# Kernel tuning notes

Hardware: AMD Instinct MI355X
Metric: run time of the kernel (lower is better)

The kernel has to match this reference:

```python
import jax, jax.numpy as jnp
import numpy as np

N = 512      # hidden states
M = 32000    # observation vocab
B = 64       # batch
TMAX = 256   # max sequence length


def setup_inputs() -> dict:
    key = jax.random.key(0)
    k1, k2, k3, k4, k5 = jax.random.split(key, 5)
    return {
        "x": jax.random.randint(k1, (B, TMAX), 0, M),          # observations
        "T": jax.random.randint(k2, (B,), 1, TMAX + 1),        # lengths in [1, TMAX]
        "trans": jax.random.normal(k3, (N, N), dtype=jnp.float32),  # unnormalized transition
        "emis": jax.random.normal(k4, (N, M), dtype=jnp.float32),   # unnormalized emission
        "prior": jax.random.normal(k5, (N,), dtype=jnp.float32),    # unnormalized state priors
    }


def reference(x, T, trans, emis, prior):
    # columns of transition matrix sum to 1 (log_softmax over dim=0 in torch)
    log_A = jax.nn.log_softmax(trans, axis=0)    # (N, N): log_A[j, k] = log p(z_t=j | z_{t-1}=k)
    log_E = jax.nn.log_softmax(emis, axis=1)     # (N, M)
    log_pi = jax.nn.log_softmax(prior, axis=0)   # (N,)

    # emission log-probs for every timestep, gathered once: (B, TMAX, N)
    em = log_E.T[x]

    alpha0 = em[:, 0, :] + log_pi                # (B, N)

    def step(alpha, em_t):
        # out[b, j] = em_t[b, j] + logsumexp_k (log_A[j, k] + alpha[b, k])
        new = em_t + jax.nn.logsumexp(alpha[:, None, :] + log_A[None, :, :], axis=2)
        return new, new

    _, alphas = jax.lax.scan(step, alpha0, jnp.swapaxes(em[:, 1:, :], 0, 1))  # (TMAX-1, B, N)
    log_alpha = jnp.concatenate([alpha0[:, None, :], jnp.swapaxes(alphas, 0, 1)], axis=1)  # (B, TMAX, N)

    log_sums = jax.nn.logsumexp(log_alpha, axis=2)                       # (B, TMAX)
    log_probs = jnp.take_along_axis(log_sums, (T - 1)[:, None], axis=1)  # (B, 1)
    return log_probs
```

## Files before the change

### kernel.cpp

```cpp
#include <hip/hip_runtime.h>
#include <math.h>

#define Nn 512
#define Mm 32000
#define Bb 64
#define Tt 256
#define NCONS 4
#define NPROD 128

typedef float v4f __attribute__((ext_vector_type(4)));
typedef float f4  __attribute__((ext_vector_type(4)));
typedef int   v4i __attribute__((ext_vector_type(4)));
typedef int   v8i __attribute__((ext_vector_type(8)));

__device__ inline int pk4fp8(float a, float b, float c, float d) {
  int r = __builtin_amdgcn_cvt_pk_fp8_f32(a, b, 0, false);
  r = __builtin_amdgcn_cvt_pk_fp8_f32(c, d, r, true);
  return r;
}

__global__ void k_colsum(const float* __restrict__ trans, float* __restrict__ colsum) {
  int tid = threadIdx.x;
  int j0 = blockIdx.x * 16;
  float a0 = 0.f, a1 = 0.f;
  for (int r = 0; r < 16; ++r) {
    a0 += __expf(trans[(j0 + r) * Nn + tid]);
    a1 += __expf(trans[(j0 + r) * Nn + 256 + tid]);
  }
  atomicAdd(&colsum[tid], a0);
  atomicAdd(&colsum[256 + tid], a1);
}

__global__ void k_writeA8(const float* __restrict__ trans, const float* __restrict__ colsum,
                          int* __restrict__ A8) {
  int d = blockIdx.x * 256 + threadIdx.x;
  int j = d >> 7, k0 = (d & 127) << 2;
  float v0 = 256.f * __expf(trans[j * Nn + k0 + 0]) / colsum[k0 + 0];
  float v1 = 256.f * __expf(trans[j * Nn + k0 + 1]) / colsum[k0 + 1];
  float v2 = 256.f * __expf(trans[j * Nn + k0 + 2]) / colsum[k0 + 2];
  float v3 = 256.f * __expf(trans[j * Nn + k0 + 3]) / colsum[k0 + 3];
  A8[d] = pk4fp8(v0, v1, v2, v3);
}

__global__ __attribute__((amdgpu_flat_work_group_size(512, 512), amdgpu_waves_per_eu(2, 2)))
void k_fused(
    const char* __restrict__ A8, const float* __restrict__ emis,
    const int* __restrict__ x, const float* __restrict__ prior,
    const int* __restrict__ Tlen, float* __restrict__ Pem2,
    int* __restrict__ progress, float* __restrict__ out)
{
  __shared__ __align__(16) char ybuf[2][16 * Nn];
  __shared__ __align__(16) float ss[512];
  __shared__ __align__(16) f4 ss4[512];
  const int tid = threadIdx.x;

  if (blockIdx.x >= NCONS) {
    const int p = blockIdx.x - NCONS;
    const int j0 = p * 4;

    float e = __expf(prior[tid]);
    ss[tid] = e; __syncthreads();
    for (int off = 256; off; off >>= 1) { if (tid < off) ss[tid] += ss[tid + off]; __syncthreads(); }
    const float ptot = ss[0];

    const f4* q0 = (const f4*)(emis + (size_t)(j0 + 0) * Mm);
    const f4* q1 = (const f4*)(emis + (size_t)(j0 + 1) * Mm);
    const f4* q2 = (const f4*)(emis + (size_t)(j0 + 2) * Mm);
    const f4* q3 = (const f4*)(emis + (size_t)(j0 + 3) * Mm);
    f4 a4 = {0.f, 0.f, 0.f, 0.f};
    for (int i = tid; i < Mm / 4; i += 512) {
      f4 v0 = q0[i], v1 = q1[i], v2 = q2[i], v3 = q3[i];
      a4[0] += (__expf(v0[0]) + __expf(v0[1])) + (__expf(v0[2]) + __expf(v0[3]));
      a4[1] += (__expf(v1[0]) + __expf(v1[1])) + (__expf(v1[2]) + __expf(v1[3]));
      a4[2] += (__expf(v2[0]) + __expf(v2[1])) + (__expf(v2[2]) + __expf(v2[3]));
      a4[3] += (__expf(v3[0]) + __expf(v3[1])) + (__expf(v3[2]) + __expf(v3[3]));
    }
    ss4[tid] = a4; __syncthreads();
    for (int off = 256; off; off >>= 1) { if (tid < off) ss4[tid] += ss4[tid + off]; __syncthreads(); }
    f4 tot = ss4[0];
    f4 rs, fz;
    #pragma unroll
    for (int q = 0; q < 4; ++q) {
      rs[q] = 32768.f / tot[q];
      fz[q] = rs[q] * 256.f * __expf(prior[j0 + q]) / ptot;
    }

    const float* r0 = emis + (size_t)(j0 + 0) * Mm;
    const float* r1 = emis + (size_t)(j0 + 1) * Mm;
    const float* r2 = emis + (size_t)(j0 + 2) * Mm;
    const float* r3 = emis + (size_t)(j0 + 3) * Mm;
    f4* P4 = (f4*)Pem2;
    for (int c8 = 0; c8 < 8; ++c8) {
      #pragma unroll
      for (int r = 0; r < 4; ++r) {
        int idx = c8 * 2048 + r * 512 + tid;
        int t = idx >> 6, b = idx & 63;
        int mv = x[b * Tt + t];
        f4 fq = (t == 0) ? fz : rs;
        f4 o = { __expf(r0[mv]) * fq[0], __expf(r1[mv]) * fq[1],
                 __expf(r2[mv]) * fq[2], __expf(r3[mv]) * fq[3] };
        P4[t * 8192 + (b >> 4) * 2048 + p * 16 + (b & 15)] = o;
      }
      __syncthreads();
      if (tid == 0) {
        __builtin_amdgcn_fence(__ATOMIC_RELEASE, "agent");
        __hip_atomic_fetch_add(&progress[c8], 1, __ATOMIC_RELAXED, __HIP_MEMORY_SCOPE_AGENT);
      }
    }
    return;
  }

  const int g = blockIdx.x;
  const int w = tid >> 6, lane = tid & 63;
  const int c = lane & 15, kq = lane >> 4;
  const int jw = w * 64;
  const int swz = (c & 7) << 4;
  const int b = g * 16 + c;

  v8i af[4][4];
  #pragma unroll
  for (int rt = 0; rt < 4; ++rt)
    #pragma unroll
    for (int kc = 0; kc < 4; ++kc)
      af[rt][kc] = *reinterpret_cast<const v8i*>(
          A8 + (size_t)(jw + rt * 16 + c) * Nn + kc * 128 + kq * 32);

  v8i onesv;
  #pragma unroll
  for (int u = 0; u < 8; ++u) onesv[u] = 0x38383838;

  #pragma unroll
  for (int rt = 0; rt < 4; ++rt)
    #pragma unroll
    for (int kc = 0; kc < 4; ++kc)
      asm volatile("" : "+v"(af[rt][kc]));
  asm volatile("" : "+v"(onesv));

  const int Tb = Tlen[b];
  int E = 23;
  int csafe = 0;

  #define ENSURE(NEED)                                                                      \
    while (csafe <= (NEED)) {                                                               \
      if (__hip_atomic_load(&progress[csafe], __ATOMIC_RELAXED,                             \
                            __HIP_MEMORY_SCOPE_AGENT) >= NPROD) {                           \
        ++csafe;                                                                            \
        __builtin_amdgcn_fence(__ATOMIC_ACQUIRE, "agent");                                  \
      } else __builtin_amdgcn_s_sleep(2);                                                   \
    }

  const int roA0 = (c * Nn + kq * 32) ^ swz;
  const int roB0 = roA0 ^ 16;
  const int wf0 = (c * Nn + jw + kq * 4) ^ swz;
  const int wf1 = wf0 ^ 16, wf2 = wf0 ^ 32, wf3 = wf0 ^ 48;
  char* const yb0 = &ybuf[0][0];

  const char* rdA_e = yb0 + roA0;
  const char* rdB_e = yb0 + roB0;
  const char* rdA_o = rdA_e + 8192;
  const char* rdB_o = rdB_e + 8192;
  char* const wb_o = yb0 + 8192;
  char* const wb_e = yb0;

  ENSURE(0);

  {
    int cc = tid & 15, grp = tid >> 4, jb = grp * 16, sz = (cc & 7) << 4;
    const f4* P0 = (const f4*)Pem2 + g * 2048 + (jb >> 2) * 16 + cc;
    #pragma unroll
    for (int q = 0; q < 4; ++q) {
      f4 v = P0[q * 16];
      *reinterpret_cast<int*>(yb0 + ((cc * Nn + jb + q * 4) ^ sz)) = pk4fp8(v[0], v[1], v[2], v[3]);
    }
  }
  __syncthreads();

  const f4* pemP = (const f4*)Pem2 + (8192 + g * 2048 + jw * 4 + kq * 16 + c);

  union BU { v8i v; v4i h[2]; };

  #define LOADMFMA(RDA, RDB)                                                                 \
    BU b0, b1, b2, b3;                                                                       \
    b0.h[0] = *(const v4i*)((RDA) + 0);   b0.h[1] = *(const v4i*)((RDB) + 0);                \
    b1.h[0] = *(const v4i*)((RDA) + 128); b1.h[1] = *(const v4i*)((RDB) + 128);              \
    b2.h[0] = *(const v4i*)((RDA) + 256); b2.h[1] = *(const v4i*)((RDB) + 256);              \
    b3.h[0] = *(const v4i*)((RDA) + 384); b3.h[1] = *(const v4i*)((RDB) + 384);              \
    v4f a0 = {0.f,0.f,0.f,0.f}, a1 = {0.f,0.f,0.f,0.f};                                     \
    v4f a2 = {0.f,0.f,0.f,0.f}, a3 = {0.f,0.f,0.f,0.f};                                     \
    v4f as_ = {0.f,0.f,0.f,0.f};                                                            \
    as_ = __builtin_amdgcn_mfma_scale_f32_16x16x128_f8f6f4(onesv,    b0.v, as_, 0,0,0, 0x7F, 0, 0x7F); \
    a0  = __builtin_amdgcn_mfma_scale_f32_16x16x128_f8f6f4(af[0][0], b0.v, a0, 0,0,0, 0x7F, 0, 0x7F); \
    a1  = __builtin_amdgcn_mfma_scale_f32_16x16x128_f8f6f4(af[1][0], b0.v, a1, 0,0,0, 0x7F, 0, 0x7F); \
    a2  = __builtin_amdgcn_mfma_scale_f32_16x16x128_f8f6f4(af[2][0], b0.v, a2, 0,0,0, 0x7F, 0, 0x7F); \
    a3  = __builtin_amdgcn_mfma_scale_f32_16x16x128_f8f6f4(af[3][0], b0.v, a3, 0,0,0, 0x7F, 0, 0x7F); \
    as_ = __builtin_amdgcn_mfma_scale_f32_16x16x128_f8f6f4(onesv,    b1.v, as_, 0,0,0, 0x7F, 0, 0x7F); \
    a0  = __builtin_amdgcn_mfma_scale_f32_16x16x128_f8f6f4(af[0][1], b1.v, a0, 0,0,0, 0x7F, 0, 0x7F); \
    a1  = __builtin_amdgcn_mfma_scale_f32_16x16x128_f8f6f4(af[1][1], b1.v, a1, 0,0,0, 0x7F, 0, 0x7F); \
    a2  = __builtin_amdgcn_mfma_scale_f32_16x16x128_f8f6f4(af[2][1], b1.v, a2, 0,0,0, 0x7F, 0, 0x7F); \
    a3  = __builtin_amdgcn_mfma_scale_f32_16x16x128_f8f6f4(af[3][1], b1.v, a3, 0,0,0, 0x7F, 0, 0x7F); \
    as_ = __builtin_amdgcn_mfma_scale_f32_16x16x128_f8f6f4(onesv,    b2.v, as_, 0,0,0, 0x7F, 0, 0x7F); \
    a0  = __builtin_amdgcn_mfma_scale_f32_16x16x128_f8f6f4(af[0][2], b2.v, a0, 0,0,0, 0x7F, 0, 0x7F); \
    a1  = __builtin_amdgcn_mfma_scale_f32_16x16x128_f8f6f4(af[1][2], b2.v, a1, 0,0,0, 0x7F, 0, 0x7F); \
    a2  = __builtin_amdgcn_mfma_scale_f32_16x16x128_f8f6f4(af[2][2], b2.v, a2, 0,0,0, 0x7F, 0, 0x7F); \
    a3  = __builtin_amdgcn_mfma_scale_f32_16x16x128_f8f6f4(af[3][2], b2.v, a3, 0,0,0, 0x7F, 0, 0x7F); \
    as_ = __builtin_amdgcn_mfma_scale_f32_16x16x128_f8f6f4(onesv,    b3.v, as_, 0,0,0, 0x7F, 0, 0x7F); \
    a0  = __builtin_amdgcn_mfma_scale_f32_16x16x128_f8f6f4(af[0][3], b3.v, a0, 0,0,0, 0x7F, 0, 0x7F); \
    a1  = __builtin_amdgcn_mfma_scale_f32_16x16x128_f8f6f4(af[1][3], b3.v, a1, 0,0,0, 0x7F, 0, 0x7F); \
    a2  = __builtin_amdgcn_mfma_scale_f32_16x16x128_f8f6f4(af[2][3], b3.v, a2, 0,0,0, 0x7F, 0, 0x7F); \
    a3  = __builtin_amdgcn_mfma_scale_f32_16x16x128_f8f6f4(af[3][3], b3.v, a3, 0,0,0, 0x7F, 0, 0x7F);

  #define EPILOG(WBASE)                                                                      \
    {                                                                                        \
      v4f scl4 = {scl, scl, scl, scl};                                                       \
      v4f v0 = a0 * (pem0 * scl4);                                                           \
      v4f v1 = a1 * (pem1 * scl4);                                                           \
      v4f v2 = a2 * (pem2 * scl4);                                                           \
      v4f v3 = a3 * (pem3 * scl4);                                                           \
      *(int*)((WBASE) + wf0) = pk4fp8(v0[0], v0[1], v0[2], v0[3]);                           \
      *(int*)((WBASE) + wf1) = pk4fp8(v1[0], v1[1], v1[2], v1[3]);                           \
      *(int*)((WBASE) + wf2) = pk4fp8(v2[0], v2[1], v2[2], v2[3]);                           \
      *(int*)((WBASE) + wf3) = pk4fp8(v3[0], v3[1], v3[2], v3[3]);                           \
    }

  for (int t = 1; t <= Tt; t += 2) {
    {
      f4 pem0 = pemP[0], pem1 = pemP[64], pem2 = pemP[128], pem3 = pemP[192];
      LOADMFMA(rdA_e, rdB_e)
      float S = as_[0];
      int expb = (int)((__float_as_uint(S) >> 23) & 0xFF);
      if (w == 0 && kq == 0 && Tb == t) out[b] = __logf(S) - (float)E * 0.69314718056f;
      E += 150 - expb;
      float scl = __uint_as_float((unsigned)(254 - expb) << 23);
      EPILOG(wb_o)
      __syncthreads();
    }
    {
      const int T = t + 1;
      if (T < Tt && (T & 31) == 0) ENSURE(T >> 5);
      f4 pem0, pem1, pem2, pem3;
      const f4* p2 = pemP + 8192;
      if (T < Tt) { pem0 = p2[0]; pem1 = p2[64]; pem2 = p2[128]; pem3 = p2[192]; }
      LOADMFMA(rdA_o, rdB_o)
      float S = as_[0];
      int expb = (int)((__float_as_uint(S) >> 23) & 0xFF);
      if (w == 0 && kq == 0 && Tb == T) out[b] = __logf(S) - (float)E * 0.69314718056f;
      if (T == Tt) goto done;
      E += 150 - expb;
      float scl = __uint_as_float((unsigned)(254 - expb) << 23);
      EPILOG(wb_e)
      __syncthreads();
    }
    pemP += 16384;
  }
done: ;
  #undef LOADMFMA
  #undef EPILOG
  #undef ENSURE
}

extern "C" void kernel_launch(void* const* d_in, const int* in_sizes, int n_in,
                              void* d_out, int out_size, void* d_ws, size_t ws_size,
                              hipStream_t stream) {
  const int*   x     = (const int*)  d_in[0];
  const int*   Tlen  = (const int*)  d_in[1];
  const float* trans = (const float*)d_in[2];
  const float* emis  = (const float*)d_in[3];
  const float* prior = (const float*)d_in[4];
  float* out = (float*)d_out;

  char* w = (char*)d_ws;
  char*  A8       = (char*)(w);
  float* colsum   = (float*)(w + (512 << 10));
  int*   progress = (int*)  (w + (512 << 10) + 4096);
  float* Pem2     = (float*)(w + (1024 << 10));

  hipMemsetAsync(w + (512 << 10), 0, 8192, stream);
  k_colsum <<<32,  256, 0, stream>>>(trans, colsum);
  k_writeA8<<<256, 256, 0, stream>>>(trans, colsum, (int*)A8);
  k_fused  <<<NCONS + NPROD, 512, 0, stream>>>(A8, emis, x, prior, Tlen, Pem2, progress, out);
}
```

Measured before the change: 291.2 us.

## Fold emission row normalization into transition matrix and precompute in wide pre-kernel

Emission row sums are moved out of the 128 producer blocks into a separate 544-block pre-kernel that also computes the transition column sums. The emission normalization factor (1/rowsum) and the prior are folded into the FP8 transition matrix and into a small pi2 vector, so producers only compute raw exp(emis) gathers. This shortens the producer critical path before the consumers can start, at the cost of a full extra pass over the 65 MB emission matrix before the fused kernel launches. It also changes FP8 scaling, since the per-row factor now multiplies A rather than the emission term, which risks range or precision issues.

```diff
diff --git a/kernel.cpp b/kernel.cpp
--- a/kernel.cpp
+++ b/kernel.cpp
@@ -19,72 +19,69 @@
   return r;
 }
 
-__global__ void k_colsum(const float* __restrict__ trans, float* __restrict__ colsum) {
-  int tid = threadIdx.x;
-  int j0 = blockIdx.x * 16;
-  float a0 = 0.f, a1 = 0.f;
-  for (int r = 0; r < 16; ++r) {
-    a0 += __expf(trans[(j0 + r) * Nn + tid]);
-    a1 += __expf(trans[(j0 + r) * Nn + 256 + tid]);
-  }
-  atomicAdd(&colsum[tid], a0);
-  atomicAdd(&colsum[256 + tid], a1);
+__global__ void k_pre(const float* __restrict__ trans, const float* __restrict__ emis,
+                      float* __restrict__ colsum, float* __restrict__ rowsum) {
+  __shared__ float ss[256];
+  const int tid = threadIdx.x, bid = blockIdx.x;
+  if (bid < 512) {
+    const f4* row4 = (const f4*)(emis + (size_t)bid * Mm);
+    float s = 0.f;
+    for (int i = tid; i < Mm / 4; i += 256) {
+      f4 v = row4[i];
+      s += (__expf(v[0]) + __expf(v[1])) + (__expf(v[2]) + __expf(v[3]));
+    }
+    ss[tid] = s; __syncthreads();
+    for (int off = 128; off; off >>= 1) { if (tid < off) ss[tid] += ss[tid + off]; __syncthreads(); }
+    if (tid == 0) rowsum[bid] = ss[0];
+  } else {
+    int j0 = (bid - 512) * 16;
+    float a0 = 0.f, a1 = 0.f;
+    for (int r = 0; r < 16; ++r) {
+      a0 += __expf(trans[(j0 + r) * Nn + tid]);
+      a1 += __expf(trans[(j0 + r) * Nn + 256 + tid]);
+    }
+    atomicAdd(&colsum[tid], a0);
+    atomicAdd(&colsum[256 + tid], a1);
+  }
 }
 
 __global__ void k_writeA8(const float* __restrict__ trans, const float* __restrict__ colsum,
-                          int* __restrict__ A8) {
-  int d = blockIdx.x * 256 + threadIdx.x;
+                          const float* __restrict__ rowsum, const float* __restrict__ prior,
+                          int* __restrict__ A8, float* __restrict__ pi2) {
+  const int tid = threadIdx.x;
+  if (blockIdx.x == 256) {
+    __shared__ float ss[256];
+    float e0 = __expf(prior[tid]), e1 = __expf(prior[tid + 256]);
+    ss[tid] = e0 + e1; __syncthreads();
+    for (int off = 128; off; off >>= 1) { if (tid < off) ss[tid] += ss[tid + off]; __syncthreads(); }
+    float ptot = ss[0];
+    pi2[tid]       = 8388608.f * e0 / (ptot * rowsum[tid]);
+    pi2[tid + 256] = 8388608.f * e1 / (ptot * rowsum[tid + 256]);
+    return;
+  }
+  int d = blockIdx.x * 256 + tid;
   int j = d >> 7, k0 = (d & 127) << 2;
-  float v0 = 256.f * __expf(trans[j * Nn + k0 + 0]) / colsum[k0 + 0];
-  float v1 = 256.f * __expf(trans[j * Nn + k0 + 1]) / colsum[k0 + 1];
-  float v2 = 256.f * __expf(trans[j * Nn + k0 + 2]) / colsum[k0 + 2];
-  float v3 = 256.f * __expf(trans[j * Nn + k0 + 3]) / colsum[k0 + 3];
+  float f = 8388608.f / rowsum[j];
+  float v0 = f * __expf(trans[j * Nn + k0 + 0]) / colsum[k0 + 0];
+  float v1 = f * __expf(trans[j * Nn + k0 + 1]) / colsum[k0 + 1];
+  float v2 = f * __expf(trans[j * Nn + k0 + 2]) / colsum[k0 + 2];
+  float v3 = f * __expf(trans[j * Nn + k0 + 3]) / colsum[k0 + 3];
   A8[d] = pk4fp8(v0, v1, v2, v3);
 }
 
 __global__ __attribute__((amdgpu_flat_work_group_size(512, 512), amdgpu_waves_per_eu(2, 2)))
 void k_fused(
     const char* __restrict__ A8, const float* __restrict__ emis,
-    const int* __restrict__ x, const float* __restrict__ prior,
+    const int* __restrict__ x, const float* __restrict__ pi2,
     const int* __restrict__ Tlen, float* __restrict__ Pem2,
     int* __restrict__ progress, float* __restrict__ out)
 {
   __shared__ __align__(16) char ybuf[2][16 * Nn];
-  __shared__ __align__(16) float ss[512];
-  __shared__ __align__(16) f4 ss4[512];
   const int tid = threadIdx.x;
 
   if (blockIdx.x >= NCONS) {
     const int p = blockIdx.x - NCONS;
     const int j0 = p * 4;
-
-    float e = __expf(prior[tid]);
-    ss[tid] = e; __syncthreads();
-    for (int off = 256; off; off >>= 1) { if (tid < off) ss[tid] += ss[tid + off]; __syncthreads(); }
-    const float ptot = ss[0];
-
-    const f4* q0 = (const f4*)(emis + (size_t)(j0 + 0) * Mm);
-    const f4* q1 = (const f4*)(emis + (size_t)(j0 + 1) * Mm);
-    const f4* q2 = (const f4*)(emis + (size_t)(j0 + 2) * Mm);
-    const f4* q3 = (const f4*)(emis + (size_t)(j0 + 3) * Mm);
-    f4 a4 = {0.f, 0.f, 0.f, 0.f};
-    for (int i = tid; i < Mm / 4; i += 512) {
-      f4 v0 = q0[i], v1 = q1[i], v2 = q2[i], v3 = q3[i];
-      a4[0] += (__expf(v0[0]) + __expf(v0[1])) + (__expf(v0[2]) + __expf(v0[3]));
-      a4[1] += (__expf(v1[0]) + __expf(v1[1])) + (__expf(v1[2]) + __expf(v1[3]));
-      a4[2] += (__expf(v2[0]) + __expf(v2[1])) + (__expf(v2[2]) + __expf(v2[3]));
-      a4[3] += (__expf(v3[0]) + __expf(v3[1])) + (__expf(v3[2]) + __expf(v3[3]));
-    }
-    ss4[tid] = a4; __syncthreads();
-    for (int off = 256; off; off >>= 1) { if (tid < off) ss4[tid] += ss4[tid + off]; __syncthreads(); }
-    f4 tot = ss4[0];
-    f4 rs, fz;
-    #pragma unroll
-    for (int q = 0; q < 4; ++q) {
-      rs[q] = 32768.f / tot[q];
-      fz[q] = rs[q] * 256.f * __expf(prior[j0 + q]) / ptot;
-    }
-
     const float* r0 = emis + (size_t)(j0 + 0) * Mm;
     const float* r1 = emis + (size_t)(j0 + 1) * Mm;
     const float* r2 = emis + (size_t)(j0 + 2) * Mm;
@@ -96,9 +93,7 @@
         int idx = c8 * 2048 + r * 512 + tid;
         int t = idx >> 6, b = idx & 63;
         int mv = x[b * Tt + t];
-        f4 fq = (t == 0) ? fz : rs;
-        f4 o = { __expf(r0[mv]) * fq[0], __expf(r1[mv]) * fq[1],
-                 __expf(r2[mv]) * fq[2], __expf(r3[mv]) * fq[3] };
+        f4 o = { __expf(r0[mv]), __expf(r1[mv]), __expf(r2[mv]), __expf(r3[mv]) };
         P4[t * 8192 + (b >> 4) * 2048 + p * 16 + (b & 15)] = o;
       }
       __syncthreads();
@@ -167,9 +162,10 @@
   {
     int cc = tid & 15, grp = tid >> 4, jb = grp * 16, sz = (cc & 7) << 4;
     const f4* P0 = (const f4*)Pem2 + g * 2048 + (jb >> 2) * 16 + cc;
+    const f4* PI = (const f4*)pi2 + (jb >> 2);
     #pragma unroll
     for (int q = 0; q < 4; ++q) {
-      f4 v = P0[q * 16];
+      f4 v = P0[q * 16] * PI[q];
       *reinterpret_cast<int*>(yb0 + ((cc * Nn + jb + q * 4) ^ sz)) = pk4fp8(v[0], v[1], v[2], v[3]);
     }
   }
@@ -271,11 +267,13 @@
   char* w = (char*)d_ws;
   char*  A8       = (char*)(w);
   float* colsum   = (float*)(w + (512 << 10));
-  int*   progress = (int*)  (w + (512 << 10) + 4096);
+  float* rowsum   = (float*)(w + (512 << 10) + 2048);
+  float* pi2      = (float*)(w + (512 << 10) + 4096);
+  int*   progress = (int*)  (w + (512 << 10) + 8192);
   float* Pem2     = (float*)(w + (1024 << 10));
 
-  hipMemsetAsync(w + (512 << 10), 0, 8192, stream);
-  k_colsum <<<32,  256, 0, stream>>>(trans, colsum);
-  k_writeA8<<<256, 256, 0, stream>>>(trans, colsum, (int*)A8);
-  k_fused  <<<NCONS + NPROD, 512, 0, stream>>>(A8, emis, x, prior, Tlen, Pem2, progress, out);
-}
+  hipMemsetAsync(w + (512 << 10), 0, 12288, stream);
+  k_pre    <<<544, 256, 0, stream>>>(trans, emis, colsum, rowsum);
+  k_writeA8<<<257, 256, 0, stream>>>(trans, colsum, rowsum, prior, (int*)A8, pi2);
+  k_fused  <<<NCONS + NPROD, 512, 0, stream>>>(A8, emis, x, pi2, Tlen, Pem2, progress, out);
+}
```

After: 295.9 us. About the same (+1.6%).

## Fuse normalization prep into one kernel and fold emission normalization into transitions

Applied to the files above, without the earlier changes.

Drops the separate column-sum and FP8 transition-writing kernels and launches a single kernel with extra prep blocks. These blocks compute the transition column sums and the emission row sums in parallel and signal completion through progress counters. Producers now write unnormalized emission probabilities. Consumers wait for the prep counters, then build the FP8 transition fragments directly in registers, folding the per-row emission normalization into the transition rows; the t=0 term is scaled separately using the prior. This removes two launches and the A8 global round-trip. The cost is that consumers spin until all 412 prep blocks finish, and correctness relies on the grid being scheduled so those blocks eventually run.

```diff
diff --git a/kernel.cpp b/kernel.cpp
--- a/kernel.cpp
+++ b/kernel.cpp
@@ -7,6 +7,7 @@
 #define Tt 256
 #define NCONS 4
 #define NPROD 128
+#define NPRE  412
 
 typedef float v4f __attribute__((ext_vector_type(4)));
 typedef float f4  __attribute__((ext_vector_type(4)));
@@ -19,72 +20,55 @@
   return r;
 }
 
-__global__ void k_colsum(const float* __restrict__ trans, float* __restrict__ colsum) {
-  int tid = threadIdx.x;
-  int j0 = blockIdx.x * 16;
-  float a0 = 0.f, a1 = 0.f;
-  for (int r = 0; r < 16; ++r) {
-    a0 += __expf(trans[(j0 + r) * Nn + tid]);
-    a1 += __expf(trans[(j0 + r) * Nn + 256 + tid]);
-  }
-  atomicAdd(&colsum[tid], a0);
-  atomicAdd(&colsum[256 + tid], a1);
-}
-
-__global__ void k_writeA8(const float* __restrict__ trans, const float* __restrict__ colsum,
-                          int* __restrict__ A8) {
-  int d = blockIdx.x * 256 + threadIdx.x;
-  int j = d >> 7, k0 = (d & 127) << 2;
-  float v0 = 256.f * __expf(trans[j * Nn + k0 + 0]) / colsum[k0 + 0];
-  float v1 = 256.f * __expf(trans[j * Nn + k0 + 1]) / colsum[k0 + 1];
-  float v2 = 256.f * __expf(trans[j * Nn + k0 + 2]) / colsum[k0 + 2];
-  float v3 = 256.f * __expf(trans[j * Nn + k0 + 3]) / colsum[k0 + 3];
-  A8[d] = pk4fp8(v0, v1, v2, v3);
-}
-
 __global__ __attribute__((amdgpu_flat_work_group_size(512, 512), amdgpu_waves_per_eu(2, 2)))
-void k_fused(
-    const char* __restrict__ A8, const float* __restrict__ emis,
+void k_all(
+    const float* __restrict__ trans, const float* __restrict__ emis,
     const int* __restrict__ x, const float* __restrict__ prior,
-    const int* __restrict__ Tlen, float* __restrict__ Pem2,
+    const int* __restrict__ Tlen, float* __restrict__ colsum,
+    float* __restrict__ rowsum, float* __restrict__ Pem2,
     int* __restrict__ progress, float* __restrict__ out)
 {
   __shared__ __align__(16) char ybuf[2][16 * Nn];
   __shared__ __align__(16) float ss[512];
-  __shared__ __align__(16) f4 ss4[512];
   const int tid = threadIdx.x;
-
-  if (blockIdx.x >= NCONS) {
-    const int p = blockIdx.x - NCONS;
+  const int bid = blockIdx.x;
+
+  if (bid >= NCONS + NPROD) {
+    const int q = bid - (NCONS + NPROD);
+    if (q < 32) {
+      int j0 = q * 16;
+      float a = 0.f;
+      #pragma unroll 4
+      for (int r = 0; r < 16; ++r) a += __expf(trans[(j0 + r) * Nn + tid]);
+      atomicAdd(&colsum[tid], a);
+      __syncthreads();
+      if (tid == 0) {
+        __builtin_amdgcn_fence(__ATOMIC_RELEASE, "agent");
+        __hip_atomic_fetch_add(&progress[9], 1, __ATOMIC_RELAXED, __HIP_MEMORY_SCOPE_AGENT);
+      }
+    }
+    for (int row = q; row < Nn; row += NPRE) {
+      const f4* r4 = (const f4*)(emis + (size_t)row * Mm);
+      float s = 0.f;
+      for (int i = tid; i < Mm / 4; i += 512) {
+        f4 v = r4[i];
+        s += (__expf(v[0]) + __expf(v[1])) + (__expf(v[2]) + __expf(v[3]));
+      }
+      ss[tid] = s; __syncthreads();
+      for (int off = 256; off; off >>= 1) { if (tid < off) ss[tid] += ss[tid + off]; __syncthreads(); }
+      if (tid == 0) rowsum[row] = ss[0];
+      __syncthreads();
+    }
+    if (tid == 0) {
+      __builtin_amdgcn_fence(__ATOMIC_RELEASE, "agent");
+      __hip_atomic_fetch_add(&progress[8], 1, __ATOMIC_RELAXED, __HIP_MEMORY_SCOPE_AGENT);
+    }
+    return;
+  }
+
+  if (bid >= NCONS) {
+    const int p = bid - NCONS;
     const int j0 = p * 4;
-
-    float e = __expf(prior[tid]);
-    ss[tid] = e; __syncthreads();
-    for (int off = 256; off; off >>= 1) { if (tid < off) ss[tid] += ss[tid + off]; __syncthreads(); }
-    const float ptot = ss[0];
-
-    const f4* q0 = (const f4*)(emis + (size_t)(j0 + 0) * Mm);
-    const f4* q1 = (const f4*)(emis + (size_t)(j0 + 1) * Mm);
-    const f4* q2 = (const f4*)(emis + (size_t)(j0 + 2) * Mm);
-    const f4* q3 = (const f4*)(emis + (size_t)(j0 + 3) * Mm);
-    f4 a4 = {0.f, 0.f, 0.f, 0.f};
-    for (int i = tid; i < Mm / 4; i += 512) {
-      f4 v0 = q0[i], v1 = q1[i], v2 = q2[i], v3 = q3[i];
-      a4[0] += (__expf(v0[0]) + __expf(v0[1])) + (__expf(v0[2]) + __expf(v0[3]));
-      a4[1] += (__expf(v1[0]) + __expf(v1[1])) + (__expf(v1[2]) + __expf(v1[3]));
-      a4[2] += (__expf(v2[0]) + __expf(v2[1])) + (__expf(v2[2]) + __expf(v2[3]));
-      a4[3] += (__expf(v3[0]) + __expf(v3[1])) + (__expf(v3[2]) + __expf(v3[3]));
-    }
-    ss4[tid] = a4; __syncthreads();
-    for (int off = 256; off; off >>= 1) { if (tid < off) ss4[tid] += ss4[tid + off]; __syncthreads(); }
-    f4 tot = ss4[0];
-    f4 rs, fz;
-    #pragma unroll
-    for (int q = 0; q < 4; ++q) {
-      rs[q] = 32768.f / tot[q];
-      fz[q] = rs[q] * 256.f * __expf(prior[j0 + q]) / ptot;
-    }
-
     const float* r0 = emis + (size_t)(j0 + 0) * Mm;
     const float* r1 = emis + (size_t)(j0 + 1) * Mm;
     const float* r2 = emis + (size_t)(j0 + 2) * Mm;
@@ -96,9 +80,7 @@
         int idx = c8 * 2048 + r * 512 + tid;
         int t = idx >> 6, b = idx & 63;
         int mv = x[b * Tt + t];
-        f4 fq = (t == 0) ? fz : rs;
-        f4 o = { __expf(r0[mv]) * fq[0], __expf(r1[mv]) * fq[1],
-                 __expf(r2[mv]) * fq[2], __expf(r3[mv]) * fq[3] };
+        f4 o = { __expf(r0[mv]), __expf(r1[mv]), __expf(r2[mv]), __expf(r3[mv]) };
         P4[t * 8192 + (b >> 4) * 2048 + p * 16 + (b & 15)] = o;
       }
       __syncthreads();
@@ -110,20 +92,49 @@
     return;
   }
 
-  const int g = blockIdx.x;
+  const int g = bid;
   const int w = tid >> 6, lane = tid & 63;
   const int c = lane & 15, kq = lane >> 4;
   const int jw = w * 64;
   const int swz = (c & 7) << 4;
   const int b = g * 16 + c;
 
+  float ptot;
+  {
+    float e = __expf(prior[tid]);
+    ss[tid] = e; __syncthreads();
+    for (int off = 256; off; off >>= 1) { if (tid < off) ss[tid] += ss[tid + off]; __syncthreads(); }
+    ptot = ss[0];
+    __syncthreads();
+  }
+
+  while (__hip_atomic_load(&progress[9], __ATOMIC_RELAXED, __HIP_MEMORY_SCOPE_AGENT) < 32 ||
+         __hip_atomic_load(&progress[8], __ATOMIC_RELAXED, __HIP_MEMORY_SCOPE_AGENT) < NPRE)
+    __builtin_amdgcn_s_sleep(2);
+  __builtin_amdgcn_fence(__ATOMIC_ACQUIRE, "agent");
+
+  ss[tid] = 1.0f / colsum[tid];
+  __syncthreads();
   v8i af[4][4];
   #pragma unroll
-  for (int rt = 0; rt < 4; ++rt)
+  for (int rt = 0; rt < 4; ++rt) {
+    int jrow = jw + rt * 16 + c;
+    float fr = 8388608.f / rowsum[jrow];
+    const float* trow = trans + (size_t)jrow * Nn;
     #pragma unroll
-    for (int kc = 0; kc < 4; ++kc)
-      af[rt][kc] = *reinterpret_cast<const v8i*>(
-          A8 + (size_t)(jw + rt * 16 + c) * Nn + kc * 128 + kq * 32);
+    for (int kc = 0; kc < 4; ++kc) {
+      int k0 = kc * 128 + kq * 32;
+      int wd[8];
+      #pragma unroll
+      for (int u = 0; u < 8; ++u) {
+        f4 tv = *(const f4*)(trow + k0 + u * 4);
+        f4 cw = *(const f4*)(&ss[k0 + u * 4]);
+        wd[u] = pk4fp8(fr * __expf(tv[0]) * cw[0], fr * __expf(tv[1]) * cw[1],
+                       fr * __expf(tv[2]) * cw[2], fr * __expf(tv[3]) * cw[3]);
+      }
+      af[rt][kc] = (v8i){wd[0], wd[1], wd[2], wd[3], wd[4], wd[5], wd[6], wd[7]};
+    }
+  }
 
   v8i onesv;
   #pragma unroll
@@ -167,10 +178,17 @@
   {
     int cc = tid & 15, grp = tid >> 4, jb = grp * 16, sz = (cc & 7) << 4;
     const f4* P0 = (const f4*)Pem2 + g * 2048 + (jb >> 2) * 16 + cc;
+    float pf = 8388608.f / ptot;
     #pragma unroll
     for (int q = 0; q < 4; ++q) {
+      int j = jb + q * 4;
+      f4 pr = *(const f4*)(prior + j);
+      f4 rw = *(const f4*)(rowsum + j);
       f4 v = P0[q * 16];
-      *reinterpret_cast<int*>(yb0 + ((cc * Nn + jb + q * 4) ^ sz)) = pk4fp8(v[0], v[1], v[2], v[3]);
+      f4 y;
+      #pragma unroll
+      for (int i = 0; i < 4; ++i) y[i] = v[i] * pf * __expf(pr[i]) / rw[i];
+      *reinterpret_cast<int*>(yb0 + ((cc * Nn + j) ^ sz)) = pk4fp8(y[0], y[1], y[2], y[3]);
     }
   }
   __syncthreads();
@@ -269,13 +287,12 @@
   float* out = (float*)d_out;
 
   char* w = (char*)d_ws;
-  char*  A8       = (char*)(w);
   float* colsum   = (float*)(w + (512 << 10));
+  float* rowsum   = (float*)(w + (512 << 10) + 2048);
   int*   progress = (int*)  (w + (512 << 10) + 4096);
   float* Pem2     = (float*)(w + (1024 << 10));
 
   hipMemsetAsync(w + (512 << 10), 0, 8192, stream);
-  k_colsum <<<32,  256, 0, stream>>>(trans, colsum);
-  k_writeA8<<<256, 256, 0, stream>>>(trans, colsum, (int*)A8);
-  k_fused  <<<NCONS + NPROD, 512, 0, stream>>>(A8, emis, x, prior, Tlen, Pem2, progress, out);
+  k_all<<<NCONS + NPROD + NPRE, 512, 0, stream>>>(trans, emis, x, prior, Tlen,
+                                                  colsum, rowsum, Pem2, progress, out);
 }
```

Result: slower. 386.7 us (+32.8%).
